# Performance work log

Hardware: AMD Instinct MI355X
Metric: run time of the kernel (lower is better)

Reference implementation:

```python
import jax, jax.numpy as jnp
import numpy as np

N_NODES = 50000
N_EDGES = 1600000
NUM_GRAPHS = 512
IN_FEATS = 128
HIDDEN = 128
NUM_CLASSES = 10
STEPS = 3


def setup_inputs() -> dict:
    key = jax.random.key(0)
    ks = jax.random.split(key, 16)
    x = jax.random.normal(ks[0], (N_NODES, IN_FEATS), dtype=jnp.float32)
    edge_index = jax.random.randint(ks[1], (2, N_EDGES), 0, N_NODES, dtype=jnp.int64)
    batch = jnp.sort(jax.random.randint(ks[2], (N_NODES,), 0, NUM_GRAPHS, dtype=jnp.int64))
    s = 0.1
    W1 = jax.random.normal(ks[3], (IN_FEATS, HIDDEN), dtype=jnp.float32) * s
    b1 = jnp.zeros((HIDDEN,), dtype=jnp.float32)
    W2 = jax.random.normal(ks[4], (HIDDEN, HIDDEN), dtype=jnp.float32) * s
    b2 = jnp.zeros((HIDDEN,), dtype=jnp.float32)
    # LSTM: input 2*HIDDEN -> hidden HIDDEN, torch gate order i,f,g,o
    Wih = jax.random.normal(ks[5], (4 * HIDDEN, 2 * HIDDEN), dtype=jnp.float32) * s
    Whh = jax.random.normal(ks[6], (4 * HIDDEN, HIDDEN), dtype=jnp.float32) * s
    bih = jnp.zeros((4 * HIDDEN,), dtype=jnp.float32)
    bhh = jnp.zeros((4 * HIDDEN,), dtype=jnp.float32)
    Wl1 = jax.random.normal(ks[7], (2 * HIDDEN, HIDDEN), dtype=jnp.float32) * s
    bl1 = jnp.zeros((HIDDEN,), dtype=jnp.float32)
    Wl2 = jax.random.normal(ks[8], (HIDDEN, NUM_CLASSES), dtype=jnp.float32) * s
    bl2 = jnp.zeros((NUM_CLASSES,), dtype=jnp.float32)
    return dict(x=x, edge_index=edge_index, batch=batch, W1=W1, b1=b1, W2=W2, b2=b2,
                Wih=Wih, Whh=Whh, bih=bih, bhh=bhh, Wl1=Wl1, bl1=bl1, Wl2=Wl2, bl2=bl2)


def gcn_conv(x, src, dst, W, b, n_nodes):
    # PyG GCNConv: add self-loops, sym-normalized scatter-add aggregation
    loop = jnp.arange(n_nodes, dtype=src.dtype)
    s = jnp.concatenate([src, loop])
    d = jnp.concatenate([dst, loop])
    deg = jax.ops.segment_sum(jnp.ones_like(d, dtype=x.dtype), d, num_segments=n_nodes)
    dinv = jnp.where(deg > 0, jax.lax.rsqrt(jnp.maximum(deg, 1.0)), 0.0)
    norm = dinv[s] * dinv[d]  # [E+N]
    h = x @ W  # [N, out]
    agg = jax.ops.segment_sum(norm[:, None] * h[s], d, num_segments=n_nodes)
    return agg + b


def segment_softmax(e, seg, num_segments):
    m = jax.ops.segment_max(e, seg, num_segments=num_segments)
    m = jnp.where(jnp.isfinite(m), m, 0.0)
    z = jnp.exp(e - m[seg])
    denom = jax.ops.segment_sum(z, seg, num_segments=num_segments)
    return z / denom[seg]


def set2set(x, batch, Wih, Whh, bih, bhh, num_graphs, steps):
    D = x.shape[1]
    h = jnp.zeros((num_graphs, D), dtype=x.dtype)
    c = jnp.zeros((num_graphs, D), dtype=x.dtype)
    q_star = jnp.zeros((num_graphs, 2 * D), dtype=x.dtype)
    for _ in range(steps):
        gates = q_star @ Wih.T + h @ Whh.T + bih + bhh  # [B, 4D]
        i, f, g, o = jnp.split(gates, 4, axis=-1)
        c = jax.nn.sigmoid(f) * c + jax.nn.sigmoid(i) * jnp.tanh(g)
        h = jax.nn.sigmoid(o) * jnp.tanh(c)
        q = h
        e = jnp.sum(x * q[batch], axis=-1)  # [N]
        a = segment_softmax(e, batch, num_graphs)
        r = jax.ops.segment_sum(a[:, None] * x, batch, num_segments=num_graphs)  # [B, D]
        q_star = jnp.concatenate([q, r], axis=-1)
    return q_star


def reference(x, edge_index, batch, W1, b1, W2, b2, Wih, Whh, bih, bhh, Wl1, bl1, Wl2, bl2):
    n = x.shape[0]
    src, dst = edge_index[0], edge_index[1]
    h = jax.nn.relu(gcn_conv(x, src, dst, W1, b1, n))
    h = jax.nn.relu(gcn_conv(h, src, dst, W2, b2, n))
    out = set2set(h, batch, Wih, Whh, bih, bhh, NUM_GRAPHS, STEPS)  # [B, 2D]
    out = jax.nn.relu(out @ Wl1 + bl1)
    return out @ Wl2 + bl2
```

## Files before the change

### kernel.cpp

```cpp
#include <hip/hip_runtime.h>
#include <hip/hip_bf16.h>
#include <math.h>

#define N_NODES 50000
#define N_EDGES 1600000
#define NUM_GRAPHS 512
#define HIDDEN 128
#define NUM_CLASSES 10
#define STEPS 3

#define NB_SHIFT 6
#define NODES_PER_B (1 << NB_SHIFT)
#define NBUK ((N_NODES + NODES_PER_B - 1) / NODES_PER_B)
#define EPB 8192
#define NBLK ((N_EDGES + EPB - 1) / EPB)
#define MAXR 144
#define NCH 7

typedef __attribute__((ext_vector_type(8))) short bf16x8;
typedef __attribute__((ext_vector_type(4))) float f32x4;

__device__ inline float bf2f(unsigned short h) {
    union { unsigned int u; float f; } v; v.u = ((unsigned int)h) << 16; return v.f;
}
__device__ inline unsigned short f2bf(float f) {
    union { float f; unsigned int u; } v; v.f = f;
    unsigned int r = (v.u + 0x7FFFu + ((v.u >> 16) & 1u)) >> 16;
    return (unsigned short)r;
}


__global__ void k_detect(const int* p, int* flag, int npairs) {
    int i = blockIdx.x * blockDim.x + threadIdx.x;
    if (i < npairs) {
        int v = p[2 * i + 1];
        if (v != 0) atomicOr(flag, 1);
    }
}

__global__ void k_goff(const void* batr, const int* flag, int* goff, int n, int ng) {
    int i = blockIdx.x * blockDim.x + threadIdx.x;
    if (i >= n) return;
    bool is32 = (*flag != 0);
    int b = is32 ? ((const int*)batr)[i] : (int)((const long long*)batr)[i];
    int prev = (i == 0) ? -1
             : (is32 ? ((const int*)batr)[i - 1] : (int)((const long long*)batr)[i - 1]);
    for (int g = prev + 1; g <= b; g++) goff[g] = i;
    if (i == n - 1) {
        for (int g = b + 1; g <= ng; g++) goff[g] = n;
    }
}

__global__ __launch_bounds__(256) void k_pack(const void* eidx, const int* flag,
                                              unsigned int* __restrict__ pdata,
                                              int* __restrict__ histg) {
    __shared__ int lh[NBUK];
    int b = blockIdx.x, t = threadIdx.x;
    for (int i = t; i < NBUK; i += 256) lh[i] = 0;
    __syncthreads();
    int base = b * EPB;
    int end = base + EPB; if (end > N_EDGES) end = N_EDGES;
    bool is32 = (*flag != 0);
    for (int i = base + t; i < end; i += 256) {
        int src, dst;
        if (is32) {
            const int* p = (const int*)eidx;
            src = p[i]; dst = p[N_EDGES + i];
        } else {
            const long long* p = (const long long*)eidx;
            src = (int)p[i]; dst = (int)p[N_EDGES + i];
        }
        pdata[i] = ((unsigned)src << 16) | (unsigned)dst;
        atomicAdd(&lh[dst >> NB_SHIFT], 1);
    }
    __syncthreads();
    for (int i = t; i < NBUK; i += 256) histg[(size_t)b * NBUK + i] = lh[i];
}

__global__ __launch_bounds__(256) void k_colscan(int* __restrict__ histg,
                                                 int* __restrict__ btot) {
    __shared__ int wsum[4];
    int k = blockIdx.x, t = threadIdx.x;
    int wid = t >> 6, lane = t & 63;
    int v = (t < NBLK) ? histg[(size_t)t * NBUK + k] : 0;
    int x = v;
#pragma unroll
    for (int o = 1; o < 64; o <<= 1) {
        int y = __shfl_up(x, o, 64);
        if (lane >= o) x += y;
    }
    if (lane == 63) wsum[wid] = x;
    __syncthreads();
    int add = 0;
    for (int w = 0; w < wid; w++) add += wsum[w];
    if (t < NBLK) histg[(size_t)t * NBUK + k] = add + x - v;
    if (t == NBLK - 1) btot[k] = add + x;
}

__global__ __launch_bounds__(1024) void k_scan(const int* cnt, int* offs, int n) {
    __shared__ int wsum[16];
    __shared__ int carry_sh;
    int t = threadIdx.x, wid = t >> 6, lane = t & 63;
    if (t == 0) { carry_sh = 0; offs[0] = 0; }
    __syncthreads();
    for (int base = 0; base < n; base += 1024) {
        int i = base + t;
        int v = (i < n) ? cnt[i] : 0;
        int x = v;
#pragma unroll
        for (int o = 1; o < 64; o <<= 1) {
            int y = __shfl_up(x, o, 64);
            if (lane >= o) x += y;
        }
        if (lane == 63) wsum[wid] = x;
        __syncthreads();
        if (wid == 0 && lane < 16) {
            int w = wsum[lane];
#pragma unroll
            for (int o = 1; o < 16; o <<= 1) {
                int y = __shfl_up(w, o, 16);
                if (lane >= o) w += y;
            }
            wsum[lane] = w;
        }
        __syncthreads();
        int add = carry_sh + (wid > 0 ? wsum[wid - 1] : 0);
        if (i < n) offs[i + 1] = add + x;
        __syncthreads();
        if (t == 0) carry_sh += wsum[15];
        __syncthreads();
    }
}

__global__ __launch_bounds__(256) void k_place(const unsigned int* __restrict__ pdata,
                                               const int* __restrict__ histg,
                                               const int* __restrict__ bbase,
                                               unsigned int* __restrict__ sdata) {
    __shared__ int lh[NBUK];
    __shared__ int lpre[NBUK];
    int b = blockIdx.x, t = threadIdx.x;
    for (int i = t; i < NBUK; i += 256) {
        lh[i] = 0;
        lpre[i] = bbase[i] + histg[(size_t)b * NBUK + i];
    }
    __syncthreads();
    int base = b * EPB;
    int end = base + EPB; if (end > N_EDGES) end = N_EDGES;
    for (int i = base + t; i < end; i += 256) {
        unsigned p = pdata[i];
        int k = (p & 0xFFFFu) >> NB_SHIFT;
        int pos = atomicAdd(&lh[k], 1);
        sdata[lpre[k] + pos] = p;
    }
}

__global__ __launch_bounds__(256) void k_build(const unsigned int* __restrict__ sdata,
                                               const int* __restrict__ bbase,
                                               const int* __restrict__ btot,
                                               float* __restrict__ dinv,
                                               int* __restrict__ offs,
                                               int* __restrict__ csr) {
    __shared__ int lc[NODES_PER_B][8];
    int b = blockIdx.x, t = threadIdx.x;
    for (int i = t; i < NODES_PER_B * 8; i += 256) ((int*)lc)[i] = 0;
    __syncthreads();
    int s0 = bbase[b], n = btot[b];
    const unsigned int* sd = sdata + s0;
    for (int e = t; e < n; e += 256) {
        unsigned p = sd[e];
        atomicAdd(&lc[p & (NODES_PER_B - 1)][(p >> 16) >> 13], 1);
    }
    __syncthreads();
    if (t < NODES_PER_B) {
        int cnts[NCH];
        int deg = 0;
#pragma unroll
        for (int c = 0; c < NCH; c++) { cnts[c] = lc[t][c]; deg += cnts[c]; }
        int x = deg;
#pragma unroll
        for (int o = 1; o < 64; o <<= 1) {
            int y = __shfl_up(x, o, 64);
            if (t >= o) x += y;
        }
        int nodestart = s0 + x - deg;
        int node = b * NODES_PER_B + t;
        if (node < N_NODES) {
            offs[node] = nodestart;
            dinv[node] = rsqrtf((float)(deg + 1));
        }
        int run = nodestart;
#pragma unroll
        for (int c = 0; c < NCH; c++) { lc[t][c] = run; run += cnts[c]; }
    }
    if (b == 0 && t == 255) offs[N_NODES] = N_EDGES;
    __syncthreads();
    for (int e = t; e < n; e += 256) {
        unsigned p = sd[e];
        int src = (int)(p >> 16);
        int pos = atomicAdd(&lc[p & (NODES_PER_B - 1)][src >> 13], 1);
        csr[pos] = src;
    }
}

__global__ void k_cvtw(const float* __restrict__ W,
                       unsigned short* __restrict__ Wth,
                       unsigned short* __restrict__ Wtl) {
    int i = blockIdx.x * 256 + threadIdx.x;
    if (i >= 128 * 128) return;
    int k = i >> 7, j = i & 127;
    float w = W[i];
    unsigned short h = f2bf(w);
    float lo = w - bf2f(h);
    Wth[j * 128 + k] = h;
    Wtl[j * 128 + k] = f2bf(lo);
}

__global__ __launch_bounds__(256) void k_gemm_mfma(const float* __restrict__ X,
                                                   const unsigned short* __restrict__ Wth,
                                                   const unsigned short* __restrict__ Wtl,
                                                   unsigned short* __restrict__ Hb,
                                                   int nrows) {
    __shared__ bf16x8 wh[2048];
    __shared__ bf16x8 wl[2048];
    int t = threadIdx.x;
    for (int i = t; i < 2048; i += 256) {
        int n = i >> 4;
        int slot = i ^ (n & 7);
        wh[slot] = ((const bf16x8*)Wth)[i];
        wl[slot] = ((const bf16x8*)Wtl)[i];
    }
    __syncthreads();
    int w = t >> 6, l = t & 63;
    int lrow = l & 15, lk = l >> 4;
    int arow = blockIdx.x * 64 + w * 16 + lrow;
    int rr = (arow < nrows) ? arow : nrows - 1;
    const float* xrow = X + (size_t)rr * 128;
    f32x4 acc[8];
#pragma unroll
    for (int nt = 0; nt < 8; nt++) acc[nt] = (f32x4){0.f, 0.f, 0.f, 0.f};
#pragma unroll
    for (int kk = 0; kk < 4; kk++) {
        int k = kk * 32 + lk * 8;
        float4 x0 = *(const float4*)(xrow + k);
        float4 x1 = *(const float4*)(xrow + k + 4);
        float xv[8] = {x0.x, x0.y, x0.z, x0.w, x1.x, x1.y, x1.z, x1.w};
        union { bf16x8 v; unsigned short s[8]; } ah, al;
#pragma unroll
        for (int i = 0; i < 8; i++) {
            unsigned u = __float_as_uint(xv[i]);
            unsigned short hi = (unsigned short)(u >> 16);
            ah.s[i] = hi;
            float lo = xv[i] - __uint_as_float((unsigned)hi << 16);
            al.s[i] = (unsigned short)(__float_as_uint(lo) >> 16);
        }
#pragma unroll
        for (int nt = 0; nt < 8; nt++) {
            int n = nt * 16 + lrow;
            int slot = (n * 16 + kk * 4 + lk) ^ (n & 7);
            bf16x8 bh = wh[slot];
            bf16x8 bl = wl[slot];
            acc[nt] = __builtin_amdgcn_mfma_f32_16x16x32_bf16(ah.v, bh, acc[nt], 0, 0, 0);
            acc[nt] = __builtin_amdgcn_mfma_f32_16x16x32_bf16(ah.v, bl, acc[nt], 0, 0, 0);
            acc[nt] = __builtin_amdgcn_mfma_f32_16x16x32_bf16(al.v, bh, acc[nt], 0, 0, 0);
        }
    }
    int obase = blockIdx.x * 64 + w * 16 + lk * 4;
#pragma unroll
    for (int r = 0; r < 4; r++) {
        int orow = obase + r;
        if (orow < nrows) {
            unsigned short* dst = Hb + (size_t)orow * 128 + lrow;
#pragma unroll
            for (int nt = 0; nt < 8; nt++) dst[nt * 16] = f2bf(acc[nt][r]);
        }
    }
}

__global__ __launch_bounds__(256) void k_agg(const unsigned short* __restrict__ Hb,
                                             const float* __restrict__ dinv,
                                             const int* __restrict__ offs,
                                             const int* __restrict__ csr,
                                             const float* __restrict__ b,
                                             float* __restrict__ out) {
    int wave = (blockIdx.x * blockDim.x + threadIdx.x) >> 6;
    int lane = threadIdx.x & 63;
    if (wave >= N_NODES) return;
    int n = wave;
    int half = lane >> 5;
    int l = lane & 31;
    float di = dinv[n];
    const ushort4* hbp = (const ushort4*)Hb;
    float4 acc = {0.f, 0.f, 0.f, 0.f};
    if (half == 0) {
        ushort4 hn = hbp[(size_t)n * 32 + l];
        acc.x = di * bf2f(hn.x); acc.y = di * bf2f(hn.y);
        acc.z = di * bf2f(hn.z); acc.w = di * bf2f(hn.w);
    }
    int e0 = offs[n], e1 = offs[n + 1];
    int j = e0 + half;
    for (; j + 14 < e1; j += 16) {
        int s[8]; float ds[8]; ushort4 a[8];
#pragma unroll
        for (int u = 0; u < 8; u++) s[u] = csr[j + 2 * u];
#pragma unroll
        for (int u = 0; u < 8; u++) ds[u] = dinv[s[u]];
#pragma unroll
        for (int u = 0; u < 8; u++) a[u] = hbp[(size_t)s[u] * 32 + l];
#pragma unroll
        for (int u = 0; u < 8; u++) {
            acc.x = fmaf(ds[u], bf2f(a[u].x), acc.x);
            acc.y = fmaf(ds[u], bf2f(a[u].y), acc.y);
            acc.z = fmaf(ds[u], bf2f(a[u].z), acc.z);
            acc.w = fmaf(ds[u], bf2f(a[u].w), acc.w);
        }
    }
    for (; j + 6 < e1; j += 8) {
        int s[4]; float ds[4]; ushort4 a[4];
#pragma unroll
        for (int u = 0; u < 4; u++) s[u] = csr[j + 2 * u];
#pragma unroll
        for (int u = 0; u < 4; u++) ds[u] = dinv[s[u]];
#pragma unroll
        for (int u = 0; u < 4; u++) a[u] = hbp[(size_t)s[u] * 32 + l];
#pragma unroll
        for (int u = 0; u < 4; u++) {
            acc.x = fmaf(ds[u], bf2f(a[u].x), acc.x);
            acc.y = fmaf(ds[u], bf2f(a[u].y), acc.y);
            acc.z = fmaf(ds[u], bf2f(a[u].z), acc.z);
            acc.w = fmaf(ds[u], bf2f(a[u].w), acc.w);
        }
    }
    for (; j < e1; j += 2) {
        int s = csr[j];
        float ds = dinv[s];
        ushort4 hs = hbp[(size_t)s * 32 + l];
        acc.x = fmaf(ds, bf2f(hs.x), acc.x); acc.y = fmaf(ds, bf2f(hs.y), acc.y);
        acc.z = fmaf(ds, bf2f(hs.z), acc.z); acc.w = fmaf(ds, bf2f(hs.w), acc.w);
    }
    acc.x += __shfl_xor(acc.x, 32, 64);
    acc.y += __shfl_xor(acc.y, 32, 64);
    acc.z += __shfl_xor(acc.z, 32, 64);
    acc.w += __shfl_xor(acc.w, 32, 64);
    if (half == 0) {
        const float4* bp = (const float4*)b;
        float4 bb = bp[l];
        float4 o4;
        o4.x = fmaxf(fmaf(di, acc.x, bb.x), 0.f);
        o4.y = fmaxf(fmaf(di, acc.y, bb.y), 0.f);
        o4.z = fmaxf(fmaf(di, acc.z, bb.z), 0.f);
        o4.w = fmaxf(fmaf(di, acc.w, bb.w), 0.f);
        ((float4*)out)[(size_t)n * 32 + l] = o4;
    }
}

__global__ __launch_bounds__(256) void k_gates(const float* __restrict__ qstar,
                                               const float* __restrict__ h,
                                               const float* __restrict__ Wih,
                                               const float* __restrict__ Whh,
                                               const float* __restrict__ bih,
                                               const float* __restrict__ bhh,
                                               float* __restrict__ gates) {
    __shared__ float As[64][33];
    __shared__ float Bs[64][33];
    int t = threadIdx.x;
    int tx = t & 15, ty = t >> 4;
    int gb = blockIdx.y * 64;
    int jb = blockIdx.x * 64;
    float acc[4][4];
#pragma unroll
    for (int i = 0; i < 4; i++)
#pragma unroll
        for (int j = 0; j < 4; j++) acc[i][j] = 0.f;
    for (int k0 = 0; k0 < 384; k0 += 32) {
        for (int i = t; i < 64 * 8; i += 256) {
            int r = i >> 3, c4 = i & 7;
            int k = k0 + c4 * 4;
            const float* srcA = (k < 256) ? (qstar + (size_t)(gb + r) * 256 + k)
                                          : (h + (size_t)(gb + r) * 128 + (k - 256));
            float4 va = *(const float4*)srcA;
            As[r][c4 * 4 + 0] = va.x; As[r][c4 * 4 + 1] = va.y;
            As[r][c4 * 4 + 2] = va.z; As[r][c4 * 4 + 3] = va.w;
            const float* srcB = (k < 256) ? (Wih + (size_t)(jb + r) * 256 + k)
                                          : (Whh + (size_t)(jb + r) * 128 + (k - 256));
            float4 vb = *(const float4*)srcB;
            Bs[r][c4 * 4 + 0] = vb.x; Bs[r][c4 * 4 + 1] = vb.y;
            Bs[r][c4 * 4 + 2] = vb.z; Bs[r][c4 * 4 + 3] = vb.w;
        }
        __syncthreads();
#pragma unroll 8
        for (int kk = 0; kk < 32; kk++) {
            float a[4], b[4];
#pragma unroll
            for (int i = 0; i < 4; i++) a[i] = As[ty * 4 + i][kk];
#pragma unroll
            for (int i = 0; i < 4; i++) b[i] = Bs[tx * 4 + i][kk];
#pragma unroll
            for (int i = 0; i < 4; i++)
#pragma unroll
                for (int j = 0; j < 4; j++) acc[i][j] = fmaf(a[i], b[j], acc[i][j]);
        }
        __syncthreads();
    }
#pragma unroll
    for (int j = 0; j < 4; j++) {
        int jj = jb + tx * 4 + j;
        float bias = bih[jj] + bhh[jj];
#pragma unroll
        for (int i = 0; i < 4; i++) {
            gates[(size_t)(gb + ty * 4 + i) * 512 + jj] = acc[i][j] + bias;
        }
    }
}

__global__ __launch_bounds__(256) void k_attn(const float* __restrict__ X,
                                              const int* __restrict__ goff,
                                              const float* __restrict__ gates,
                                              const float* __restrict__ bih,
                                              const float* __restrict__ bhh,
                                              float* __restrict__ h,
                                              float* __restrict__ c,
                                              float* __restrict__ eg,
                                              float* __restrict__ qstar,
                                              int first) {
    int b = blockIdx.x;
    int t = threadIdx.x;
    int wv = t >> 6, l = t & 63;
    int n0 = goff[b], n1 = goff[b + 1];
    int cnt = n1 - n0;
    __shared__ float rows[MAXR][128];
    __shared__ float q[128];
    __shared__ float ebuf[MAXR];
    __shared__ float red[256];
    __shared__ float wm[4];
    if (t < 128) {
        float iv, fv, gv, ov;
        if (first) {
            iv = bih[t] + bhh[t];
            fv = bih[128 + t] + bhh[128 + t];
            gv = bih[256 + t] + bhh[256 + t];
            ov = bih[384 + t] + bhh[384 + t];
        } else {
            const float* g = gates + (size_t)b * 512;
            iv = g[t]; fv = g[128 + t]; gv = g[256 + t]; ov = g[384 + t];
        }
        float si = 1.f / (1.f + expf(-iv));
        float sf = 1.f / (1.f + expf(-fv));
        float so = 1.f / (1.f + expf(-ov));
        float tg = tanhf(gv);
        float cold = first ? 0.f : c[b * 128 + t];
        float cn = sf * cold + si * tg;
        float hn = so * tanhf(cn);
        c[b * 128 + t] = cn;
        h[b * 128 + t] = hn;
        q[t] = hn;
    }
    if (cnt <= MAXR) {
        for (int i = t; i < cnt * 32; i += 256) {
            int r = i >> 5, c4 = i & 31;
            ((float4*)rows[r])[c4] = ((const float4*)(X + (size_t)(n0 + r) * 128))[c4];
        }
        __syncthreads();
        const float2* qp = (const float2*)q;
        float2 q2 = qp[l];
        float mloc = -INFINITY;
        for (int n = wv; n < cnt; n += 4) {
            const float2* xp = (const float2*)rows[n];
            float2 x2 = xp[l];
            float p = x2.x * q2.x + x2.y * q2.y;
#pragma unroll
            for (int o = 32; o > 0; o >>= 1) p += __shfl_xor(p, o, 64);
            if (l == 0) ebuf[n] = p;
            mloc = fmaxf(mloc, p);
        }
        if (l == 0) wm[wv] = mloc;
        __syncthreads();
        float m = fmaxf(fmaxf(wm[0], wm[1]), fmaxf(wm[2], wm[3]));
        if (isinf(m)) m = 0.f;
        float s = 0.f;
        for (int n = t; n < cnt; n += 256) {
            float z = expf(ebuf[n] - m);
            ebuf[n] = z;
            s += z;
        }
        red[t] = s;
        __syncthreads();
        for (int o = 128; o > 0; o >>= 1) {
            if (t < o) red[t] += red[t + o];
            __syncthreads();
        }
        float denom = red[0];
        float inv = (denom > 0.f) ? 1.f / denom : 0.f;
        __syncthreads();
        int g = t >> 7, col = t & 127;
        float acc = 0.f;
        for (int n = g; n < cnt; n += 2) {
            acc = fmaf(ebuf[n] * inv, rows[n][col], acc);
        }
        red[t] = acc;
        __syncthreads();
        if (t < 128) {
            float r = red[t] + red[t + 128];
            qstar[b * 256 + t] = q[t];
            qstar[b * 256 + 128 + t] = r;
        }
    } else {
        __syncthreads();
        const float2* qp = (const float2*)q;
        float2 q2 = qp[l];
        float mloc = -INFINITY;
        for (int n = n0 + wv; n < n1; n += 4) {
            const float2* xp = (const float2*)(X + (size_t)n * 128);
            float2 x2 = xp[l];
            float p = x2.x * q2.x + x2.y * q2.y;
#pragma unroll
            for (int o = 32; o > 0; o >>= 1) p += __shfl_xor(p, o, 64);
            if (l == 0) eg[n] = p;
            mloc = fmaxf(mloc, p);
        }
        if (l == 0) wm[wv] = mloc;
        __syncthreads();
        float m = fmaxf(fmaxf(wm[0], wm[1]), fmaxf(wm[2], wm[3]));
        if (isinf(m)) m = 0.f;
        float s = 0.f;
        for (int n = n0 + t; n < n1; n += 256) {
            float z = expf(eg[n] - m);
            eg[n] = z;
            s += z;
        }
        red[t] = s;
        __syncthreads();
        for (int o = 128; o > 0; o >>= 1) {
            if (t < o) red[t] += red[t + o];
            __syncthreads();
        }
        float denom = red[0];
        float inv = (denom > 0.f) ? 1.f / denom : 0.f;
        __syncthreads();
        int g = t >> 7, col = t & 127;
        float acc = 0.f;
        for (int n = n0 + g; n < n1; n += 2) {
            acc = fmaf(eg[n] * inv, X[(size_t)n * 128 + col], acc);
        }
        red[t] = acc;
        __syncthreads();
        if (t < 128) {
            float r = red[t] + red[t + 128];
            qstar[b * 256 + t] = q[t];
            qstar[b * 256 + 128 + t] = r;
        }
    }
}

__global__ __launch_bounds__(128) void k_mlp(const float* __restrict__ qstar,
                                             const float* __restrict__ Wl1,
                                             const float* __restrict__ bl1,
                                             const float* __restrict__ Wl2,
                                             const float* __restrict__ bl2,
                                             float* __restrict__ out) {
    int b = blockIdx.x, t = threadIdx.x;
    __shared__ float qs[256];
    __shared__ float hid[128];
    qs[t] = qstar[b * 256 + t];
    qs[128 + t] = qstar[b * 256 + 128 + t];
    __syncthreads();
    float acc = bl1[t];
#pragma unroll 4
    for (int k = 0; k < 256; k++) acc = fmaf(qs[k], Wl1[k * 128 + t], acc);
    hid[t] = fmaxf(acc, 0.f);
    __syncthreads();
    if (t < NUM_CLASSES) {
        float o = bl2[t];
#pragma unroll 4
        for (int k = 0; k < 128; k++) o = fmaf(hid[k], Wl2[k * 10 + t], o);
        out[b * 10 + t] = o;
    }
}


extern "C" void kernel_launch(void* const* d_in, const int* in_sizes, int n_in,
                              void* d_out, int out_size, void* d_ws, size_t ws_size,
                              hipStream_t stream) {
    const float* x    = (const float*)d_in[0];
    const void*  eidx = d_in[1];
    const void*  batr = d_in[2];
    const float* W1   = (const float*)d_in[3];
    const float* b1   = (const float*)d_in[4];
    const float* W2   = (const float*)d_in[5];
    const float* b2   = (const float*)d_in[6];
    const float* Wih  = (const float*)d_in[7];
    const float* Whh  = (const float*)d_in[8];
    const float* bih  = (const float*)d_in[9];
    const float* bhh  = (const float*)d_in[10];
    const float* Wl1  = (const float*)d_in[11];
    const float* bl1  = (const float*)d_in[12];
    const float* Wl2  = (const float*)d_in[13];
    const float* bl2  = (const float*)d_in[14];
    float* out = (float*)d_out;

    char* ws = (char*)d_ws;
    size_t off = 0;
    auto alloc = [&](size_t bytes) {
        size_t r = off;
        off = (off + bytes + 255) & ~(size_t)255;
        return r;
    };
    float* A        = (float*)(ws + alloc((size_t)N_NODES * 128 * 4));
    int*   csr      = (int*)(ws + alloc((size_t)N_EDGES * 4));
    unsigned int* edgebuf = (unsigned int*)(ws + alloc((size_t)2 * N_EDGES * 4));
    int*   histg    = (int*)(ws + alloc((size_t)NBLK * NBUK * 4));
    int*   btot     = (int*)(ws + alloc((size_t)NBUK * 4));
    int*   bbase    = (int*)(ws + alloc((size_t)(NBUK + 1) * 4));
    int*   offs     = (int*)(ws + alloc((size_t)(N_NODES + 1) * 4));
    float* dinv     = (float*)(ws + alloc((size_t)N_NODES * 4));
    float* e        = (float*)(ws + alloc((size_t)N_NODES * 4));
    int*   goff     = (int*)(ws + alloc((size_t)(NUM_GRAPHS + 1) * 4));
    float* state    = (float*)(ws + alloc((size_t)(NUM_GRAPHS * 128 * 2 + NUM_GRAPHS * 256) * 4));
    float* gates    = (float*)(ws + alloc((size_t)NUM_GRAPHS * 512 * 4));
    unsigned short* Wth1 = (unsigned short*)(ws + alloc((size_t)128 * 128 * 2));
    unsigned short* Wtl1 = (unsigned short*)(ws + alloc((size_t)128 * 128 * 2));
    unsigned short* Wth2 = (unsigned short*)(ws + alloc((size_t)128 * 128 * 2));
    unsigned short* Wtl2 = (unsigned short*)(ws + alloc((size_t)128 * 128 * 2));
    int*   flag     = (int*)(ws + alloc(4));
    if (off > ws_size) return;

    unsigned int* pdata = edgebuf;
    unsigned int* sdata = edgebuf + N_EDGES;
    unsigned short* Hb = (unsigned short*)edgebuf;

    float* h_lstm = state;
    float* c_lstm = state + NUM_GRAPHS * 128;
    float* qstar  = state + NUM_GRAPHS * 256;

    const int B = 256;
    hipMemsetAsync(flag, 0, 4, stream);
    k_detect<<<(4096 + B - 1) / B, B, 0, stream>>>((const int*)eidx, flag, 4096);
    k_goff<<<(N_NODES + B - 1) / B, B, 0, stream>>>(batr, flag, goff, N_NODES, NUM_GRAPHS);
    k_pack<<<NBLK, 256, 0, stream>>>(eidx, flag, pdata, histg);
    k_colscan<<<NBUK, 256, 0, stream>>>(histg, btot);
    k_scan<<<1, 1024, 0, stream>>>(btot, bbase, NBUK);
    k_place<<<NBLK, 256, 0, stream>>>(pdata, histg, bbase, sdata);
    k_build<<<NBUK, 256, 0, stream>>>(sdata, bbase, btot, dinv, offs, csr);
    k_cvtw<<<64, 256, 0, stream>>>(W1, Wth1, Wtl1);
    k_cvtw<<<64, 256, 0, stream>>>(W2, Wth2, Wtl2);
    k_gemm_mfma<<<(N_NODES + 63) / 64, 256, 0, stream>>>(x, Wth1, Wtl1, Hb, N_NODES);
    k_agg<<<(N_NODES + 3) / 4, 256, 0, stream>>>(Hb, dinv, offs, csr, b1, A);
    k_gemm_mfma<<<(N_NODES + 63) / 64, 256, 0, stream>>>(A, Wth2, Wtl2, Hb, N_NODES);
    k_agg<<<(N_NODES + 3) / 4, 256, 0, stream>>>(Hb, dinv, offs, csr, b2, A);
    for (int s = 0; s < STEPS; s++) {
        if (s > 0) {
            dim3 gg(8, 8);
            k_gates<<<gg, 256, 0, stream>>>(qstar, h_lstm, Wih, Whh, bih, bhh, gates);
        }
        k_attn<<<NUM_GRAPHS, 256, 0, stream>>>(A, goff, gates, bih, bhh,
                                               h_lstm, c_lstm, e, qstar, s == 0);
    }
    k_mlp<<<NUM_GRAPHS, 128, 0, stream>>>(qstar, Wl1, bl1, Wl2, bl2, out);
}
```

Before: 361.8 us.

## Pre-scale GEMM output by dinv, use 16-bit CSR, widen aggregation loads

The GEMM epilogue now multiplies each row by its source dinv before storing bf16, so the aggregation no longer gathers dinv per edge. CSR source indices are stored as 16-bit values, which halves index traffic. Each node's aggregation now uses quarter-wave groups with 16-byte loads in place of half-wave groups with 8-byte loads. Node ids above 65535 would overflow the 16-bit index; with 50000 nodes this fits. Rounding to bf16 after the scaling changes numerics slightly.

```diff
diff --git a/kernel.cpp b/kernel.cpp
--- a/kernel.cpp
+++ b/kernel.cpp
@@ -18,6 +18,7 @@
 #define NCH 7
 
 typedef __attribute__((ext_vector_type(8))) short bf16x8;
+typedef __attribute__((ext_vector_type(8))) unsigned short u16x8;
 typedef __attribute__((ext_vector_type(4))) float f32x4;
 
 __device__ inline float bf2f(unsigned short h) {
@@ -159,7 +160,7 @@
                                                const int* __restrict__ btot,
                                                float* __restrict__ dinv,
                                                int* __restrict__ offs,
-                                               int* __restrict__ csr) {
+                                               unsigned short* __restrict__ csr) {
     __shared__ int lc[NODES_PER_B][8];
     int b = blockIdx.x, t = threadIdx.x;
     for (int i = t; i < NODES_PER_B * 8; i += 256) ((int*)lc)[i] = 0;
@@ -198,7 +199,7 @@
         unsigned p = sd[e];
         int src = (int)(p >> 16);
         int pos = atomicAdd(&lc[p & (NODES_PER_B - 1)][src >> 13], 1);
-        csr[pos] = src;
+        csr[pos] = (unsigned short)src;
     }
 }
 
@@ -218,6 +219,7 @@
 __global__ __launch_bounds__(256) void k_gemm_mfma(const float* __restrict__ X,
                                                    const unsigned short* __restrict__ Wth,
                                                    const unsigned short* __restrict__ Wtl,
+                                                   const float* __restrict__ dinv,
                                                    unsigned short* __restrict__ Hb,
                                                    int nrows) {
     __shared__ bf16x8 wh[2048];
@@ -269,87 +271,80 @@
     for (int r = 0; r < 4; r++) {
         int orow = obase + r;
         if (orow < nrows) {
+            float di = dinv[orow];
             unsigned short* dst = Hb + (size_t)orow * 128 + lrow;
 #pragma unroll
-            for (int nt = 0; nt < 8; nt++) dst[nt * 16] = f2bf(acc[nt][r]);
-        }
-    }
-}
-
-__global__ __launch_bounds__(256) void k_agg(const unsigned short* __restrict__ Hb,
+            for (int nt = 0; nt < 8; nt++) dst[nt * 16] = f2bf(di * acc[nt][r]);
+        }
+    }
+}
+
+__global__ __launch_bounds__(256) void k_agg(const unsigned short* __restrict__ Hbs,
                                              const float* __restrict__ dinv,
                                              const int* __restrict__ offs,
-                                             const int* __restrict__ csr,
+                                             const unsigned short* __restrict__ csr,
                                              const float* __restrict__ b,
                                              float* __restrict__ out) {
     int wave = (blockIdx.x * blockDim.x + threadIdx.x) >> 6;
     int lane = threadIdx.x & 63;
     if (wave >= N_NODES) return;
     int n = wave;
-    int half = lane >> 5;
-    int l = lane & 31;
-    float di = dinv[n];
-    const ushort4* hbp = (const ushort4*)Hb;
-    float4 acc = {0.f, 0.f, 0.f, 0.f};
-    if (half == 0) {
-        ushort4 hn = hbp[(size_t)n * 32 + l];
-        acc.x = di * bf2f(hn.x); acc.y = di * bf2f(hn.y);
-        acc.z = di * bf2f(hn.z); acc.w = di * bf2f(hn.w);
+    int qr = lane >> 4;
+    int l = lane & 15;
+    const u16x8* hp = (const u16x8*)Hbs;
+    float acc[8];
+    if (qr == 0) {
+        u16x8 hv = hp[(size_t)n * 16 + l];
+#pragma unroll
+        for (int i = 0; i < 8; i++) acc[i] = bf2f(hv[i]);
+    } else {
+#pragma unroll
+        for (int i = 0; i < 8; i++) acc[i] = 0.f;
     }
     int e0 = offs[n], e1 = offs[n + 1];
-    int j = e0 + half;
-    for (; j + 14 < e1; j += 16) {
-        int s[8]; float ds[8]; ushort4 a[8];
-#pragma unroll
-        for (int u = 0; u < 8; u++) s[u] = csr[j + 2 * u];
-#pragma unroll
-        for (int u = 0; u < 8; u++) ds[u] = dinv[s[u]];
-#pragma unroll
-        for (int u = 0; u < 8; u++) a[u] = hbp[(size_t)s[u] * 32 + l];
-#pragma unroll
-        for (int u = 0; u < 8; u++) {
-            acc.x = fmaf(ds[u], bf2f(a[u].x), acc.x);
-            acc.y = fmaf(ds[u], bf2f(a[u].y), acc.y);
-            acc.z = fmaf(ds[u], bf2f(a[u].z), acc.z);
-            acc.w = fmaf(ds[u], bf2f(a[u].w), acc.w);
-        }
-    }
-    for (; j + 6 < e1; j += 8) {
-        int s[4]; float ds[4]; ushort4 a[4];
-#pragma unroll
-        for (int u = 0; u < 4; u++) s[u] = csr[j + 2 * u];
-#pragma unroll
-        for (int u = 0; u < 4; u++) ds[u] = dinv[s[u]];
-#pragma unroll
-        for (int u = 0; u < 4; u++) a[u] = hbp[(size_t)s[u] * 32 + l];
-#pragma unroll
-        for (int u = 0; u < 4; u++) {
-            acc.x = fmaf(ds[u], bf2f(a[u].x), acc.x);
-            acc.y = fmaf(ds[u], bf2f(a[u].y), acc.y);
-            acc.z = fmaf(ds[u], bf2f(a[u].z), acc.z);
-            acc.w = fmaf(ds[u], bf2f(a[u].w), acc.w);
-        }
-    }
-    for (; j < e1; j += 2) {
+    int j = e0 + qr;
+    for (; j + 12 < e1; j += 16) {
+        int s0 = csr[j], s1 = csr[j + 4], s2 = csr[j + 8], s3 = csr[j + 12];
+        u16x8 a0 = hp[(size_t)s0 * 16 + l];
+        u16x8 a1 = hp[(size_t)s1 * 16 + l];
+        u16x8 a2 = hp[(size_t)s2 * 16 + l];
+        u16x8 a3 = hp[(size_t)s3 * 16 + l];
+#pragma unroll
+        for (int i = 0; i < 8; i++) acc[i] += bf2f(a0[i]);
+#pragma unroll
+        for (int i = 0; i < 8; i++) acc[i] += bf2f(a1[i]);
+#pragma unroll
+        for (int i = 0; i < 8; i++) acc[i] += bf2f(a2[i]);
+#pragma unroll
+        for (int i = 0; i < 8; i++) acc[i] += bf2f(a3[i]);
+    }
+    for (; j < e1; j += 4) {
         int s = csr[j];
-        float ds = dinv[s];
-        ushort4 hs = hbp[(size_t)s * 32 + l];
-        acc.x = fmaf(ds, bf2f(hs.x), acc.x); acc.y = fmaf(ds, bf2f(hs.y), acc.y);
-        acc.z = fmaf(ds, bf2f(hs.z), acc.z); acc.w = fmaf(ds, bf2f(hs.w), acc.w);
-    }
-    acc.x += __shfl_xor(acc.x, 32, 64);
-    acc.y += __shfl_xor(acc.y, 32, 64);
-    acc.z += __shfl_xor(acc.z, 32, 64);
-    acc.w += __shfl_xor(acc.w, 32, 64);
-    if (half == 0) {
-        const float4* bp = (const float4*)b;
-        float4 bb = bp[l];
-        float4 o4;
-        o4.x = fmaxf(fmaf(di, acc.x, bb.x), 0.f);
-        o4.y = fmaxf(fmaf(di, acc.y, bb.y), 0.f);
-        o4.z = fmaxf(fmaf(di, acc.z, bb.z), 0.f);
-        o4.w = fmaxf(fmaf(di, acc.w, bb.w), 0.f);
-        ((float4*)out)[(size_t)n * 32 + l] = o4;
+        u16x8 a = hp[(size_t)s * 16 + l];
+#pragma unroll
+        for (int i = 0; i < 8; i++) acc[i] += bf2f(a[i]);
+    }
+#pragma unroll
+    for (int i = 0; i < 8; i++) {
+        acc[i] += __shfl_xor(acc[i], 16, 64);
+        acc[i] += __shfl_xor(acc[i], 32, 64);
+    }
+    if (qr == 0) {
+        float di = dinv[n];
+        float4 b0 = *(const float4*)(b + l * 8);
+        float4 b1 = *(const float4*)(b + l * 8 + 4);
+        float4 o0, o1;
+        o0.x = fmaxf(fmaf(di, acc[0], b0.x), 0.f);
+        o0.y = fmaxf(fmaf(di, acc[1], b0.y), 0.f);
+        o0.z = fmaxf(fmaf(di, acc[2], b0.z), 0.f);
+        o0.w = fmaxf(fmaf(di, acc[3], b0.w), 0.f);
+        o1.x = fmaxf(fmaf(di, acc[4], b1.x), 0.f);
+        o1.y = fmaxf(fmaf(di, acc[5], b1.y), 0.f);
+        o1.z = fmaxf(fmaf(di, acc[6], b1.z), 0.f);
+        o1.w = fmaxf(fmaf(di, acc[7], b1.w), 0.f);
+        float* dst = out + (size_t)n * 128 + l * 8;
+        *(float4*)dst = o0;
+        *(float4*)(dst + 4) = o1;
     }
 }
 
@@ -605,7 +600,7 @@
         return r;
     };
     float* A        = (float*)(ws + alloc((size_t)N_NODES * 128 * 4));
-    int*   csr      = (int*)(ws + alloc((size_t)N_EDGES * 4));
+    unsigned short* csr = (unsigned short*)(ws + alloc((size_t)N_EDGES * 2));
     unsigned int* edgebuf = (unsigned int*)(ws + alloc((size_t)2 * N_EDGES * 4));
     int*   histg    = (int*)(ws + alloc((size_t)NBLK * NBUK * 4));
     int*   btot     = (int*)(ws + alloc((size_t)NBUK * 4));
@@ -625,7 +620,7 @@
 
     unsigned int* pdata = edgebuf;
     unsigned int* sdata = edgebuf + N_EDGES;
-    unsigned short* Hb = (unsigned short*)edgebuf;
+    unsigned short* Hbs = (unsigned short*)edgebuf;
 
     float* h_lstm = state;
     float* c_lstm = state + NUM_GRAPHS * 128;
@@ -642,10 +637,10 @@
     k_build<<<NBUK, 256, 0, stream>>>(sdata, bbase, btot, dinv, offs, csr);
     k_cvtw<<<64, 256, 0, stream>>>(W1, Wth1, Wtl1);
     k_cvtw<<<64, 256, 0, stream>>>(W2, Wth2, Wtl2);
-    k_gemm_mfma<<<(N_NODES + 63) / 64, 256, 0, stream>>>(x, Wth1, Wtl1, Hb, N_NODES);
-    k_agg<<<(N_NODES + 3) / 4, 256, 0, stream>>>(Hb, dinv, offs, csr, b1, A);
-    k_gemm_mfma<<<(N_NODES + 63) / 64, 256, 0, stream>>>(A, Wth2, Wtl2, Hb, N_NODES);
-    k_agg<<<(N_NODES + 3) / 4, 256, 0, stream>>>(Hb, dinv, offs, csr, b2, A);
+    k_gemm_mfma<<<(N_NODES + 63) / 64, 256, 0, stream>>>(x, Wth1, Wtl1, dinv, Hbs, N_NODES);
+    k_agg<<<(N_NODES + 3) / 4, 256, 0, stream>>>(Hbs, dinv, offs, csr, b1, A);
+    k_gemm_mfma<<<(N_NODES + 63) / 64, 256, 0, stream>>>(A, Wth2, Wtl2, dinv, Hbs, N_NODES);
+    k_agg<<<(N_NODES + 3) / 4, 256, 0, stream>>>(Hbs, dinv, offs, csr, b2, A);
     for (int s = 0; s < STEPS; s++) {
         if (s > 0) {
             dim3 gg(8, 8);
```

Result: no change. 356.7 us (-1.4%).
